# Kernel optimization log

Hardware: AMD Instinct MI355X
Metric: run time of the kernel (lower is better)

The kernel has to match this reference:

```python
import jax, jax.numpy as jnp
import numpy as np

NEG_INF = -9.0e15  # matches torch's -9000000000000000.0 mask value
ALPHA = 0.2        # leaky_relu negative slope
F_OUT = 128


def setup_inputs() -> dict:
    key = jax.random.key(0)
    k1, k2, k3, k4 = jax.random.split(key, 4)
    B, N, F_IN = 4, 4096, 128
    x = jax.random.normal(k1, (B, N, F_IN), dtype=jnp.float32)
    adj = jax.random.randint(k2, (B, N, N), 0, 2, dtype=jnp.int32)
    # xavier-uniform-like init for params
    lim_W = float(np.sqrt(6.0 / (F_IN + F_OUT)))
    W = jax.random.uniform(k3, (F_IN, F_OUT), jnp.float32, -lim_W, lim_W)
    lim_a = float(np.sqrt(6.0 / (2 * F_OUT + 1)))
    a = jax.random.uniform(k4, (2 * F_OUT, 1), jnp.float32, -lim_a, lim_a)
    return {"x": x, "adj": adj, "W": W, "a": a}


def reference(x, adj, W, a):
    # x: [B, N, Fin], adj: [B, N, N], W: [Fin, Fout], a: [2*Fout, 1]
    Wh = jnp.matmul(x, W)                       # [B, N, Fout]
    Wh1 = jnp.matmul(Wh, a[:F_OUT, :])          # [B, N, 1]
    Wh2 = jnp.matmul(Wh, a[F_OUT:, :])          # [B, N, 1]
    # NOTE: faithful to the source: e = Wh1 + Wh2 is [B, N, 1] (no transpose)
    e = jax.nn.leaky_relu(Wh1 + Wh2, negative_slope=ALPHA)
    # broadcast e across last dim of adj, mask, row-softmax over axis 2
    scores = jnp.where(adj > 0, e, jnp.float32(NEG_INF))  # [B, N, N]
    attention = jax.nn.softmax(scores, axis=2)
    # dropout with p=0.0 / eval mode -> identity
    h_prime = jnp.matmul(attention, Wh)         # [B, N, Fout]
    return h_prime
```

## Files before the change

### kernel.cpp

```cpp
#include <hip/hip_runtime.h>
#include <hip/hip_bf16.h>

typedef unsigned short u16;
typedef unsigned int u32;
typedef short bf16x8 __attribute__((ext_vector_type(8)));
typedef float f32x4 __attribute__((ext_vector_type(4)));

__device__ inline float bf2f(u16 u) { return __uint_as_float(((u32)u) << 16); }
__device__ inline u16 f2bf(float f) {
    u32 x = __float_as_uint(f);
    return (u16)((x + 0x7FFFu + ((x >> 16) & 1u)) >> 16);
}

__global__ __launch_bounds__(256) void k_gemm1(const float* __restrict__ x,
                                               const float* __restrict__ W,
                                               u16* __restrict__ Wht) {
    __shared__ __align__(16) u16 Wt[128][136];
    const int t = threadIdx.x;
    {
        int k = t >> 1;
        int f0 = (t & 1) * 64;
        const float4* wp = reinterpret_cast<const float4*>(W + k * 128 + f0);
#pragma unroll
        for (int q = 0; q < 16; ++q) {
            float4 v = wp[q];
            int f = f0 + q * 4;
            Wt[f + 0][k] = f2bf(v.x);
            Wt[f + 1][k] = f2bf(v.y);
            Wt[f + 2][k] = f2bf(v.z);
            Wt[f + 3][k] = f2bf(v.w);
        }
    }
    __syncthreads();

    const int w = t >> 6, l = t & 63;
    const int lr = l & 15, lg = l >> 4;
    const int fh = (w & 1) * 64;
    const int jh = (w >> 1) * 64;
    const int j0 = blockIdx.x * 128;

    f32x4 acc[4][4];
#pragma unroll
    for (int m = 0; m < 4; ++m)
#pragma unroll
        for (int n = 0; n < 4; ++n) acc[m][n] = (f32x4){0.f, 0.f, 0.f, 0.f};

#pragma unroll
    for (int ks = 0; ks < 4; ++ks) {
        bf16x8 a[4], bb[4];
#pragma unroll
        for (int m = 0; m < 4; ++m)
            a[m] = *reinterpret_cast<const bf16x8*>(&Wt[fh + m * 16 + lr][ks * 32 + lg * 8]);
#pragma unroll
        for (int n = 0; n < 4; ++n) {
            int j = j0 + jh + n * 16 + lr;
            const float* xp = x + (size_t)j * 128 + ks * 32 + lg * 8;
            float4 v0 = *reinterpret_cast<const float4*>(xp);
            float4 v1 = *reinterpret_cast<const float4*>(xp + 4);
            bf16x8 bv;
            bv[0] = (short)f2bf(v0.x); bv[1] = (short)f2bf(v0.y);
            bv[2] = (short)f2bf(v0.z); bv[3] = (short)f2bf(v0.w);
            bv[4] = (short)f2bf(v1.x); bv[5] = (short)f2bf(v1.y);
            bv[6] = (short)f2bf(v1.z); bv[7] = (short)f2bf(v1.w);
            bb[n] = bv;
        }
#pragma unroll
        for (int m = 0; m < 4; ++m)
#pragma unroll
            for (int n = 0; n < 4; ++n)
                acc[m][n] = __builtin_amdgcn_mfma_f32_16x16x32_bf16(a[m], bb[n], acc[m][n], 0, 0, 0);
    }

    const int bb_ = blockIdx.x >> 5;
    const int jj = (blockIdx.x & 31) * 128;
    u16* base = Wht + ((size_t)bb_ << 19);
#pragma unroll
    for (int m = 0; m < 4; ++m) {
        int f = fh + m * 16 + lg * 4;
#pragma unroll
        for (int n = 0; n < 4; ++n) {
            int j = jj + jh + n * 16 + lr;
#pragma unroll
            for (int r = 0; r < 4; ++r)
                base[(size_t)(f + r) * 4096 + j] = f2bf(acc[m][n][r]);
        }
    }
}

__global__ __launch_bounds__(64) void k_colsum(const u16* __restrict__ Wht,
                                               float* __restrict__ S) {
    const int row = blockIdx.x;
    const uint4* p = reinterpret_cast<const uint4*>(Wht + (size_t)row * 4096);
    const int l = threadIdx.x;
    float s = 0.f;
#pragma unroll
    for (int q = 0; q < 8; ++q) {
        uint4 v = p[l * 8 + q];
        u32 arr[4] = {v.x, v.y, v.z, v.w};
#pragma unroll
        for (int e = 0; e < 4; ++e)
            s += bf2f((u16)(arr[e] & 0xFFFFu)) + bf2f((u16)(arr[e] >> 16));
    }
#pragma unroll
    for (int off = 32; off; off >>= 1) s += __shfl_xor(s, off);
    if (l == 0) S[row] = s;
}

__global__ __launch_bounds__(256) void k_gemm2(const int* __restrict__ adj,
                                               const u16* __restrict__ Wht,
                                               const float* __restrict__ S,
                                               float* __restrict__ out) {
    __shared__ __align__(16) u16 As[2][64][72];
    __shared__ __align__(16) u16 Bs[2][128][72];
    __shared__ int cnt_lds[64];
    __shared__ float inv_lds[64];

    const int t = threadIdx.x;
    const int b = blockIdx.x >> 6;
    const int i0 = (blockIdx.x & 63) * 64;
    const int* adjb = adj + ((size_t)b << 24) + (size_t)i0 * 4096;
    const u16* whb = Wht + ((size_t)b << 19);

    const int ai = t >> 2;
    const int ak = (t & 3) * 16;
    const int bf = t >> 1;
    const int bk = (t & 1) * 32;

    int4 av[4];
    uint4 bv[4];
    int cnt = 0;

    auto issue = [&](int k0) {
        const int4* ap = reinterpret_cast<const int4*>(adjb + (size_t)ai * 4096 + k0 + ak);
        av[0] = ap[0]; av[1] = ap[1]; av[2] = ap[2]; av[3] = ap[3];
        const uint4* bp = reinterpret_cast<const uint4*>(whb + (size_t)bf * 4096 + k0 + bk);
        bv[0] = bp[0]; bv[1] = bp[1]; bv[2] = bp[2]; bv[3] = bp[3];
    };
    auto convert_write = [&](int buf) {
        u32 u[8];
#pragma unroll
        for (int q = 0; q < 4; ++q) {
            int4 v = av[q];
            u32 e0 = (v.x > 0) ? 0x3F80u : 0u;
            u32 e1 = (v.y > 0) ? 0x3F80u : 0u;
            u32 e2 = (v.z > 0) ? 0x3F80u : 0u;
            u32 e3 = (v.w > 0) ? 0x3F80u : 0u;
            cnt += (v.x > 0) + (v.y > 0) + (v.z > 0) + (v.w > 0);
            u[q * 2 + 0] = e0 | (e1 << 16);
            u[q * 2 + 1] = e2 | (e3 << 16);
        }
        uint4* aw = reinterpret_cast<uint4*>(&As[buf][ai][ak]);
        aw[0] = make_uint4(u[0], u[1], u[2], u[3]);
        aw[1] = make_uint4(u[4], u[5], u[6], u[7]);
        uint4* bw = reinterpret_cast<uint4*>(&Bs[buf][bf][bk]);
        bw[0] = bv[0]; bw[1] = bv[1]; bw[2] = bv[2]; bw[3] = bv[3];
    };

    const int w = t >> 6, l = t & 63;
    const int lr = l & 15, lg = l >> 4;
    const int ir0 = (w >> 1) * 2;
    const int fr0 = (w & 1) * 4;

    f32x4 acc[2][4];
#pragma unroll
    for (int m = 0; m < 2; ++m)
#pragma unroll
        for (int n = 0; n < 4; ++n) acc[m][n] = (f32x4){0.f, 0.f, 0.f, 0.f};

    issue(0);
    convert_write(0);
    __syncthreads();

    for (int kt = 0; kt < 64; ++kt) {
        const int cur = kt & 1;
        const bool pre = (kt + 1 < 64);
        if (pre) issue((kt + 1) * 64);

#pragma unroll
        for (int ks = 0; ks < 2; ++ks) {
            bf16x8 a[2], bb[4];
#pragma unroll
            for (int m = 0; m < 2; ++m)
                a[m] = *reinterpret_cast<const bf16x8*>(&As[cur][(ir0 + m) * 16 + lr][ks * 32 + lg * 8]);
#pragma unroll
            for (int n = 0; n < 4; ++n)
                bb[n] = *reinterpret_cast<const bf16x8*>(&Bs[cur][(fr0 + n) * 16 + lr][ks * 32 + lg * 8]);
#pragma unroll
            for (int m = 0; m < 2; ++m)
#pragma unroll
                for (int n = 0; n < 4; ++n)
                    acc[m][n] = __builtin_amdgcn_mfma_f32_16x16x32_bf16(a[m], bb[n], acc[m][n], 0, 0, 0);
        }

        if (pre) convert_write(cur ^ 1);
        __syncthreads();
    }

    int c2 = cnt + __shfl_xor(cnt, 1);
    int c4 = c2 + __shfl_xor(c2, 2);
    if ((t & 3) == 0) cnt_lds[ai] = c4;
    __syncthreads();
    if (t < 64) {
        int c = cnt_lds[t];
        inv_lds[t] = (c > 0) ? (1.0f / (float)c) : 0.0f;
    }
    __syncthreads();

    float* ob = out + (((size_t)b * 4096) + i0) * 128;
#pragma unroll
    for (int m = 0; m < 2; ++m) {
#pragma unroll
        for (int n = 0; n < 4; ++n) {
            int f = (fr0 + n) * 16 + lr;
#pragma unroll
            for (int r = 0; r < 4; ++r) {
                int il = (ir0 + m) * 16 + lg * 4 + r;
                int c = cnt_lds[il];
                float v;
                if (c > 0) v = acc[m][n][r] * inv_lds[il];
                else       v = S[b * 128 + f] * (1.0f / 4096.0f);
                ob[(size_t)il * 128 + f] = v;
            }
        }
    }
}

extern "C" void kernel_launch(void* const* d_in, const int* in_sizes, int n_in,
                              void* d_out, int out_size, void* d_ws, size_t ws_size,
                              hipStream_t stream) {
    const float* x = (const float*)d_in[0];
    const int* adj = (const int*)d_in[1];
    const float* W = (const float*)d_in[2];
    float* out = (float*)d_out;

    u16* Wht = (u16*)d_ws;
    float* S = (float*)((char*)d_ws + (size_t)4 * 128 * 4096 * 2);

    k_gemm1<<<128, 256, 0, stream>>>(x, W, Wht);
    k_colsum<<<512, 64, 0, stream>>>(Wht, S);
    k_gemm2<<<256, 256, 0, stream>>>(adj, Wht, S, out);
}
```

Baseline: 428.2 us.

## Halve gemm2 row tile, swizzle blocks, fuse column sums into gemm1

```diff
diff --git a/kernel.cpp b/kernel.cpp
--- a/kernel.cpp
+++ b/kernel.cpp
@@ -14,7 +14,8 @@
 
 __global__ __launch_bounds__(256) void k_gemm1(const float* __restrict__ x,
                                                const float* __restrict__ W,
-                                               u16* __restrict__ Wht) {
+                                               u16* __restrict__ Wht,
+                                               float* __restrict__ S) {
     __shared__ __align__(16) u16 Wt[128][136];
     const int t = threadIdx.x;
     {
@@ -74,6 +75,7 @@
     const int bb_ = blockIdx.x >> 5;
     const int jj = (blockIdx.x & 31) * 128;
     u16* base = Wht + ((size_t)bb_ << 19);
+    float* Sb = S + bb_ * 128;
 #pragma unroll
     for (int m = 0; m < 4; ++m) {
         int f = fh + m * 16 + lg * 4;
@@ -84,88 +86,74 @@
             for (int r = 0; r < 4; ++r)
                 base[(size_t)(f + r) * 4096 + j] = f2bf(acc[m][n][r]);
         }
-    }
-}
-
-__global__ __launch_bounds__(64) void k_colsum(const u16* __restrict__ Wht,
-                                               float* __restrict__ S) {
-    const int row = blockIdx.x;
-    const uint4* p = reinterpret_cast<const uint4*>(Wht + (size_t)row * 4096);
-    const int l = threadIdx.x;
-    float s = 0.f;
-#pragma unroll
-    for (int q = 0; q < 8; ++q) {
-        uint4 v = p[l * 8 + q];
-        u32 arr[4] = {v.x, v.y, v.z, v.w};
-#pragma unroll
-        for (int e = 0; e < 4; ++e)
-            s += bf2f((u16)(arr[e] & 0xFFFFu)) + bf2f((u16)(arr[e] >> 16));
-    }
-#pragma unroll
-    for (int off = 32; off; off >>= 1) s += __shfl_xor(s, off);
-    if (l == 0) S[row] = s;
+#pragma unroll
+        for (int r = 0; r < 4; ++r) {
+            float sj = 0.f;
+#pragma unroll
+            for (int n = 0; n < 4; ++n) sj += acc[m][n][r];
+            sj += __shfl_xor(sj, 1);
+            sj += __shfl_xor(sj, 2);
+            sj += __shfl_xor(sj, 4);
+            sj += __shfl_xor(sj, 8);
+            if (lr == 0) atomicAdd(&Sb[f + r], sj);
+        }
+    }
 }
 
 __global__ __launch_bounds__(256) void k_gemm2(const int* __restrict__ adj,
                                                const u16* __restrict__ Wht,
                                                const float* __restrict__ S,
                                                float* __restrict__ out) {
-    __shared__ __align__(16) u16 As[2][64][72];
+    __shared__ __align__(16) u16 As[2][32][72];
     __shared__ __align__(16) u16 Bs[2][128][72];
-    __shared__ int cnt_lds[64];
-    __shared__ float inv_lds[64];
+    __shared__ int cnt_lds[32];
+    __shared__ float inv_lds[32];
 
     const int t = threadIdx.x;
-    const int b = blockIdx.x >> 6;
-    const int i0 = (blockIdx.x & 63) * 64;
+    const int raw = blockIdx.x;
+    const int swz = (raw & 7) * 64 + (raw >> 3);
+    const int b = swz >> 7;
+    const int i0 = (swz & 127) * 32;
     const int* adjb = adj + ((size_t)b << 24) + (size_t)i0 * 4096;
     const u16* whb = Wht + ((size_t)b << 19);
 
-    const int ai = t >> 2;
-    const int ak = (t & 3) * 16;
+    const int ai = t >> 3;
+    const int ak = (t & 7) * 8;
     const int bf = t >> 1;
     const int bk = (t & 1) * 32;
 
-    int4 av[4];
+    int4 av[2];
     uint4 bv[4];
     int cnt = 0;
 
     auto issue = [&](int k0) {
         const int4* ap = reinterpret_cast<const int4*>(adjb + (size_t)ai * 4096 + k0 + ak);
-        av[0] = ap[0]; av[1] = ap[1]; av[2] = ap[2]; av[3] = ap[3];
+        av[0] = ap[0]; av[1] = ap[1];
         const uint4* bp = reinterpret_cast<const uint4*>(whb + (size_t)bf * 4096 + k0 + bk);
         bv[0] = bp[0]; bv[1] = bp[1]; bv[2] = bp[2]; bv[3] = bp[3];
     };
     auto convert_write = [&](int buf) {
-        u32 u[8];
-#pragma unroll
-        for (int q = 0; q < 4; ++q) {
+        u32 u[4];
+#pragma unroll
+        for (int q = 0; q < 2; ++q) {
             int4 v = av[q];
-            u32 e0 = (v.x > 0) ? 0x3F80u : 0u;
-            u32 e1 = (v.y > 0) ? 0x3F80u : 0u;
-            u32 e2 = (v.z > 0) ? 0x3F80u : 0u;
-            u32 e3 = (v.w > 0) ? 0x3F80u : 0u;
             cnt += (v.x > 0) + (v.y > 0) + (v.z > 0) + (v.w > 0);
-            u[q * 2 + 0] = e0 | (e1 << 16);
-            u[q * 2 + 1] = e2 | (e3 << 16);
-        }
-        uint4* aw = reinterpret_cast<uint4*>(&As[buf][ai][ak]);
-        aw[0] = make_uint4(u[0], u[1], u[2], u[3]);
-        aw[1] = make_uint4(u[4], u[5], u[6], u[7]);
+            u[q * 2 + 0] = ((v.x > 0) ? 0x3F80u : 0u) | (((v.y > 0) ? 0x3F80u : 0u) << 16);
+            u[q * 2 + 1] = ((v.z > 0) ? 0x3F80u : 0u) | (((v.w > 0) ? 0x3F80u : 0u) << 16);
+        }
+        *reinterpret_cast<uint4*>(&As[buf][ai][ak]) = make_uint4(u[0], u[1], u[2], u[3]);
         uint4* bw = reinterpret_cast<uint4*>(&Bs[buf][bf][bk]);
         bw[0] = bv[0]; bw[1] = bv[1]; bw[2] = bv[2]; bw[3] = bv[3];
     };
 
     const int w = t >> 6, l = t & 63;
     const int lr = l & 15, lg = l >> 4;
-    const int ir0 = (w >> 1) * 2;
-    const int fr0 = (w & 1) * 4;
-
-    f32x4 acc[2][4];
-#pragma unroll
-    for (int m = 0; m < 2; ++m)
-#pragma unroll
-        for (int n = 0; n < 4; ++n) acc[m][n] = (f32x4){0.f, 0.f, 0.f, 0.f};
+    const int ir = w & 1;
+    const int fr0 = (w >> 1) * 4;
+
+    f32x4 acc[4];
+#pragma unroll
+    for (int n = 0; n < 4; ++n) acc[n] = (f32x4){0.f, 0.f, 0.f, 0.f};
 
     issue(0);
     convert_write(0);
@@ -178,49 +166,40 @@
 
 #pragma unroll
         for (int ks = 0; ks < 2; ++ks) {
-            bf16x8 a[2], bb[4];
-#pragma unroll
-            for (int m = 0; m < 2; ++m)
-                a[m] = *reinterpret_cast<const bf16x8*>(&As[cur][(ir0 + m) * 16 + lr][ks * 32 + lg * 8]);
-#pragma unroll
-            for (int n = 0; n < 4; ++n)
-                bb[n] = *reinterpret_cast<const bf16x8*>(&Bs[cur][(fr0 + n) * 16 + lr][ks * 32 + lg * 8]);
-#pragma unroll
-            for (int m = 0; m < 2; ++m)
-#pragma unroll
-                for (int n = 0; n < 4; ++n)
-                    acc[m][n] = __builtin_amdgcn_mfma_f32_16x16x32_bf16(a[m], bb[n], acc[m][n], 0, 0, 0);
+            bf16x8 a = *reinterpret_cast<const bf16x8*>(&As[cur][ir * 16 + lr][ks * 32 + lg * 8]);
+#pragma unroll
+            for (int n = 0; n < 4; ++n) {
+                bf16x8 bbv = *reinterpret_cast<const bf16x8*>(&Bs[cur][(fr0 + n) * 16 + lr][ks * 32 + lg * 8]);
+                acc[n] = __builtin_amdgcn_mfma_f32_16x16x32_bf16(a, bbv, acc[n], 0, 0, 0);
+            }
         }
 
         if (pre) convert_write(cur ^ 1);
         __syncthreads();
     }
 
-    int c2 = cnt + __shfl_xor(cnt, 1);
-    int c4 = c2 + __shfl_xor(c2, 2);
-    if ((t & 3) == 0) cnt_lds[ai] = c4;
-    __syncthreads();
-    if (t < 64) {
-        int c = cnt_lds[t];
-        inv_lds[t] = (c > 0) ? (1.0f / (float)c) : 0.0f;
+    int c = cnt + __shfl_xor(cnt, 1);
+    c += __shfl_xor(c, 2);
+    c += __shfl_xor(c, 4);
+    if ((t & 7) == 0) cnt_lds[ai] = c;
+    __syncthreads();
+    if (t < 32) {
+        int cc = cnt_lds[t];
+        inv_lds[t] = (cc > 0) ? (1.0f / (float)cc) : 0.0f;
     }
     __syncthreads();
 
     float* ob = out + (((size_t)b * 4096) + i0) * 128;
 #pragma unroll
-    for (int m = 0; m < 2; ++m) {
-#pragma unroll
-        for (int n = 0; n < 4; ++n) {
-            int f = (fr0 + n) * 16 + lr;
-#pragma unroll
-            for (int r = 0; r < 4; ++r) {
-                int il = (ir0 + m) * 16 + lg * 4 + r;
-                int c = cnt_lds[il];
-                float v;
-                if (c > 0) v = acc[m][n][r] * inv_lds[il];
-                else       v = S[b * 128 + f] * (1.0f / 4096.0f);
-                ob[(size_t)il * 128 + f] = v;
-            }
+    for (int n = 0; n < 4; ++n) {
+        int f = (fr0 + n) * 16 + lr;
+        float sv = S[b * 128 + f] * (1.0f / 4096.0f);
+#pragma unroll
+        for (int r = 0; r < 4; ++r) {
+            int il = ir * 16 + lg * 4 + r;
+            int cc = cnt_lds[il];
+            float v = (cc > 0) ? acc[n][r] * inv_lds[il] : sv;
+            ob[(size_t)il * 128 + f] = v;
         }
     }
 }
@@ -236,7 +215,7 @@
     u16* Wht = (u16*)d_ws;
     float* S = (float*)((char*)d_ws + (size_t)4 * 128 * 4096 * 2);
 
-    k_gemm1<<<128, 256, 0, stream>>>(x, W, Wht);
-    k_colsum<<<512, 64, 0, stream>>>(Wht, S);
-    k_gemm2<<<256, 256, 0, stream>>>(adj, Wht, S, out);
-}
+    hipMemsetAsync(S, 0, 512 * sizeof(float), stream);
+    k_gemm1<<<128, 256, 0, stream>>>(x, W, Wht, S);
+    k_gemm2<<<512, 256, 0, stream>>>(adj, Wht, S, out);
+}
```

Result: slower. 478.0 us (+11.6%).
